# Performance work log

Measured on AMD Instinct MI355X. Metric: run time of the kernel, lower is better.

## Reference

```python
import jax, jax.numpy as jnp
import numpy as np

B = 16           # number of graphs
H = 8            # heads
NC = 9           # num_coeffs = (lmax+1)^2
DM = 128         # d_model (sphere_channels)
F = NC * DM      # flat_dim = 1152
HD = F // H      # head_dim = 144
RD = 16          # rope_dim
EPS = 1e-5


def setup_inputs() -> dict:
    key = jax.random.key(0)
    ks = jax.random.split(key, 8)
    N = 8192
    x_emb = jax.random.normal(ks[0], (N, NC, DM), dtype=jnp.float32)
    batch = jnp.sort(jax.random.randint(ks[1], (N,), 0, B)).astype(jnp.int32)
    pos = jax.random.normal(ks[2], (N, 3), dtype=jnp.float32) * 3.0
    Wqkv = jax.random.normal(ks[3], (F, 3 * F), dtype=jnp.float32) / np.sqrt(F)
    Wout = jax.random.normal(ks[4], (F, F), dtype=jnp.float32) / np.sqrt(F)
    rope_freqs = jax.random.normal(ks[5], (RD,), dtype=jnp.float32) * 0.1
    Wrope = jax.random.normal(ks[6], (RD, H), dtype=jnp.float32) / np.sqrt(RD)
    gamma = jnp.ones((F,), dtype=jnp.float32)
    beta = jnp.zeros((F,), dtype=jnp.float32)
    return {"x_emb": x_emb, "pos": pos, "Wqkv": Wqkv, "Wout": Wout,
            "rope_freqs": rope_freqs, "Wrope": Wrope,
            "gamma": gamma, "beta": beta, "batch": batch}


def _pad_layout(batch, N):
    # sorted batch ids -> per-node rank within its graph, sizes per graph
    sizes = jnp.bincount(batch, length=B)                       # [B]
    offsets = jnp.concatenate([jnp.zeros((1,), sizes.dtype), jnp.cumsum(sizes)[:-1]])
    rank = jnp.arange(N, dtype=sizes.dtype) - offsets[batch]    # [N]
    n_max = int(np.asarray(jax.device_get(sizes)).max())        # concrete pad width
    return sizes, rank, n_max


def reference(x_emb, pos, Wqkv, Wout, rope_freqs, Wrope, gamma, beta, batch):
    N = x_emb.shape[0]
    x_flat = x_emb.reshape(N, F)
    sizes, rank, n_max = _pad_layout(batch, N)

    # dense padding  [B, N_max, *]; mask True = padding slot
    x_pad = jnp.zeros((B, n_max, F), x_flat.dtype).at[batch, rank].set(x_flat)
    pos_pad = jnp.zeros((B, n_max, 3), pos.dtype).at[batch, rank].set(pos)
    mask = jnp.arange(n_max)[None, :] >= sizes[:, None]         # [B, N_max]

    qkv = x_pad @ Wqkv                                          # [B, N_max, 3F]
    q, k, v = jnp.split(qkv, 3, axis=-1)
    def heads(t):
        return t.reshape(B, n_max, H, HD).transpose(0, 2, 1, 3)  # [B,H,N_max,HD]
    q, k, v = heads(q), heads(k), heads(v)

    scale = HD ** (-0.5)
    attn = jnp.einsum('bhid,bhjd->bhij', q, k) * scale          # [B,H,N,N]

    # Fourier distance bias
    diff = pos_pad[:, :, None, :] - pos_pad[:, None, :, :]      # [B,N,N,3]
    dist = jnp.linalg.norm(diff, axis=-1)                       # [B,N,N]
    fourier = jnp.cos(dist[..., None] * jnp.abs(rope_freqs))    # [B,N,N,RD]
    bias = jnp.einsum('bijr,rh->bhij', fourier, Wrope)          # [B,H,N,N]
    pad_mask = mask[:, None, :] | mask[:, :, None]              # [B,N,N]
    bias = jnp.where(pad_mask[:, None, :, :], 0.0, bias)
    attn = attn + bias

    attn = jnp.where(mask[:, None, None, :], -jnp.inf, attn)    # key mask
    attn = jax.nn.softmax(attn, axis=-1)
    attn = jnp.nan_to_num(attn)

    out = jnp.einsum('bhij,bhjd->bhid', attn, v)                # [B,H,N,HD]
    out = out.transpose(0, 2, 1, 3).reshape(B, n_max, F) @ Wout
    out_flat = out[batch, rank]                                 # gather back [N,F]

    h = x_flat + out_flat
    mu = jnp.mean(h, axis=-1, keepdims=True)
    var = jnp.var(h, axis=-1, keepdims=True)
    y = (h - mu) / jnp.sqrt(var + EPS) * gamma + beta
    return y.reshape(N, NC, DM)
```

## Files before the change

kernel.cpp:

```cpp
#include <hip/hip_runtime.h>

typedef unsigned short u16;
typedef unsigned int   u32;
typedef __attribute__((ext_vector_type(8)))  __bf16 bf16x8;
typedef __attribute__((ext_vector_type(4)))  float  f32x4;
typedef __attribute__((ext_vector_type(16))) float  f32x16;
typedef __attribute__((ext_vector_type(4)))  u32    u32x4;

#define F_DIM   1152
#define QKV_DIM 3456
#define HD_SCALE 0.083333333333333333f
#define LOG2E    1.4426950408889634f
#define KSC      (HD_SCALE*LOG2E)
#define MAX4    80
#define BIAS_BLKS 2048

static __device__ __forceinline__ u16 f2bf(float f){
    u32 u = __builtin_bit_cast(u32, f);
    u32 r = u + 0x7fffu + ((u >> 16) & 1u);
    return (u16)(r >> 16);
}
static __device__ __forceinline__ u32 cvtpk(float lo, float hi){
    u32 r;
    asm("v_cvt_pk_bf16_f32 %0, %1, %2" : "=v"(r) : "v"(lo), "v"(hi));
    return r;
}

typedef __attribute__((address_space(1))) void gvoid;
typedef __attribute__((address_space(3))) void lvoid;
static __device__ __forceinline__ void gload16(const u16* g, u16* l){
    __builtin_amdgcn_global_load_lds((gvoid*)g, (lvoid*)l, 16, 0, 0);
}

__global__ __launch_bounds__(256) void prep_kernel(
        const float* __restrict__ x, u16* __restrict__ xb, int nCast, int n4,
        const float* __restrict__ Wqkv, u16* __restrict__ wqkvT,
        const float* __restrict__ Wout, u16* __restrict__ woutT,
        const float* __restrict__ pos, const float* __restrict__ rfreq,
        const float* __restrict__ Wrope, u16* __restrict__ biasP,
        const int* __restrict__ batch, int* __restrict__ meta, int N){
    __shared__ float tile[32][33];
    __shared__ int goffs[17];
    __shared__ int bpre[17];
    const int b = blockIdx.x, t = threadIdx.x;
    const int T1 = (QKV_DIM/32)*(F_DIM/32);
    const int T2 = (F_DIM/32)*(F_DIM/32);

    if (b < BIAS_BLKS){
        if (t <= 16){
            int lo = 0, hi = N;
            while (lo < hi){ int mid = (lo+hi)>>1; if (batch[mid] < t) lo = mid+1; else hi = mid; }
            goffs[t] = lo;
        }
        __syncthreads();
        if (t == 0){
            int bc = 0;
            for (int g = 0; g < 16; g++){
                bpre[g] = bc;
                int ng = goffs[g+1] - goffs[g];
                int ntg = (ng + 31) >> 5;
                bc += ntg*ntg;
            }
            bpre[16] = bc;
        }
        __syncthreads();
        float absf[16], w[16][8];
        #pragma unroll
        for (int r = 0; r < 16; r++){
            absf[r] = fabsf(rfreq[r]);
            #pragma unroll
            for (int h = 0; h < 8; h++) w[r][h] = Wrope[r*8 + h] * LOG2E;
        }
        const int total = bpre[16];
        for (int bb = b; bb < total; bb += BIAS_BLKS){
            int g = 0;
            while (bpre[g+1] <= bb) g++;
            int rem  = bb - bpre[g];
            int goff = goffs[g];
            int ng   = goffs[g+1] - goff;
            int ntg  = (ng + 31) >> 5;
            int qt   = rem / ntg;
            int jt   = rem - qt*ntg;
            size_t base = (size_t)bb * 8192;
            #pragma unroll
            for (int pp = 0; pp < 4; pp++){
                int p = t + pp*256;
                int i = p >> 5, c = p & 31;
                int p4 = c & 15;
                int j  = (p4 & 3) + ((p4 >> 2) << 3) + ((c >> 4) << 2);
                int qn = goff + qt*32 + i;  if (qn >= goff + ng) qn = goff + ng - 1;
                int kn = goff + jt*32 + j;  if (kn >= goff + ng) kn = goff + ng - 1;
                float dx = pos[qn*3+0] - pos[kn*3+0];
                float dy = pos[qn*3+1] - pos[kn*3+1];
                float dz = pos[qn*3+2] - pos[kn*3+2];
                float d  = sqrtf(dx*dx + dy*dy + dz*dz);
                float bv[8];
                #pragma unroll
                for (int h = 0; h < 8; h++) bv[h] = 0.f;
                #pragma unroll
                for (int r = 0; r < 16; r++){
                    float cs = __cosf(d * absf[r]);
                    #pragma unroll
                    for (int h = 0; h < 8; h++) bv[h] = fmaf(cs, w[r][h], bv[h]);
                }
                #pragma unroll
                for (int h = 0; h < 8; h++)
                    biasP[base + h*1024 + p] = f2bf(bv[h]);
            }
        }
        return;
    }
    const int b2 = b - BIAS_BLKS;
    if (b2 < nCast){
        int i = b2*256 + t;
        if (i < n4){
            float4 v = ((const float4*)x)[i];
            ((ushort4*)xb)[i] = make_ushort4(f2bf(v.x), f2bf(v.y), f2bf(v.z), f2bf(v.w));
        }
        return;
    }
    if (b2 < nCast + T1 + T2){
        const float* in; u16* out; int R, C, bi;
        if (b2 < nCast + T1){ in = Wqkv; out = wqkvT; R = F_DIM; C = QKV_DIM; bi = b2 - nCast; }
        else                { in = Wout; out = woutT; R = F_DIM; C = F_DIM;  bi = b2 - nCast - T1; }
        int gx = C/32;
        int c0 = (bi % gx)*32, r0 = (bi / gx)*32;
        int tx = t & 31, ty = t >> 5;
        #pragma unroll
        for (int yy = ty; yy < 32; yy += 8)
            tile[yy][tx] = in[(size_t)(r0+yy)*C + (c0+tx)];
        __syncthreads();
        #pragma unroll
        for (int yy = ty; yy < 32; yy += 8)
            out[(size_t)(c0+yy)*R + (r0+tx)] = f2bf(tile[tx][yy]);
        return;
    }
    if (t <= 16){
        int lo = 0, hi = N;
        while (lo < hi){ int mid = (lo+hi)>>1; if (batch[mid] < t) lo = mid+1; else hi = mid; }
        meta[1+t] = lo;
    }
    __syncthreads();
    if (t == 0){
        int ps = 0, bcnt = 0, cnt4 = 0;
        for (int g = 0; g < 16; g++){
            int ng = meta[2+g] - meta[1+g];
            meta[20+g] = ps;
            meta[40+g] = bcnt;
            int nt = (ng + 31) / 32;
            ps += nt * 32;
            bcnt += nt * nt;
            int nt4 = (nt + 3) / 4;
            for (int q4 = 0; q4 < nt4; q4++){
                meta[64 + cnt4] = g;
                meta[64 + MAX4 + cnt4] = q4;
                cnt4++;
            }
        }
        meta[36] = ps;
        meta[56] = bcnt;
        meta[0]  = cnt4;
    }
}

template<bool OUT_BF16>
__global__ __launch_bounds__(512, 2) void gemm256(const u16* __restrict__ A,
                                                  const u16* __restrict__ Bt,
                                                  void* __restrict__ Cp,
                                                  int M, int Ncols, int K){
    __shared__ u16 sA[4][8192];
    __shared__ u16 sB[4][8192];
    const int nwg = gridDim.x;
    int orig = blockIdx.x;
    int qq = nwg >> 3, rr = nwg & 7;
    int xcd = orig & 7, pos = orig >> 3;
    int nid = (xcd < rr ? xcd*(qq+1) : rr*(qq+1) + (xcd-rr)*qq) + pos;
    const int gx = M >> 8;
    const int bm = (nid % gx) << 8, bn = (nid / gx) << 8;

    const int tid = threadIdx.x;
    const int w = tid >> 6, lane = tid & 63;
    const int wr = w >> 2, wc = w & 3;
    const int fr = lane & 15, fq = lane >> 4;
    const int swz8 = (fq ^ ((fr >> 1) & 3)) * 8;

    const u16* aS[2]; const u16* bS[2]; int dOf[2];
    #pragma unroll
    for (int p = 0; p < 2; p++){
        int idx = p*512 + tid;
        int row = idx >> 2, c = idx & 3;
        int sc = c ^ ((row >> 1) & 3);
        int brow = bn + row; if (brow > Ncols-1) brow = Ncols-1;
        aS[p] = A  + (size_t)(bm + row)*K + sc*8;
        bS[p] = Bt + (size_t)brow*K + sc*8;
        dOf[p] = idx*8;
    }

    f32x4 acc[8][4];
    #pragma unroll
    for (int m = 0; m < 8; m++)
        #pragma unroll
        for (int n = 0; n < 4; n++)
            #pragma unroll
            for (int e = 0; e < 4; e++) acc[m][n][e] = 0.f;

    const int nk = K >> 5;
    #pragma unroll
    for (int p = 0; p < 2; p++){ gload16(aS[p], &sA[0][dOf[p]]); gload16(bS[p], &sB[0][dOf[p]]); }
    #pragma unroll
    for (int p = 0; p < 2; p++){ gload16(aS[p]+32, &sA[1][dOf[p]]); gload16(bS[p]+32, &sB[1][dOf[p]]); }

    #pragma unroll 1
    for (int t = 0; t < nk; t++){
        int tp = (t+2 < nk) ? t+2 : nk-1;
        int bufS = (t+2) & 3;
        #pragma unroll
        for (int p = 0; p < 2; p++){
            gload16(aS[p] + tp*32, &sA[bufS][dOf[p]]);
            gload16(bS[p] + tp*32, &sB[bufS][dOf[p]]);
        }
        asm volatile("s_waitcnt vmcnt(8)\n\ts_barrier" ::: "memory");

        const u16* sAc = &sA[t & 3][0];
        const u16* sBc = &sB[t & 3][0];
        bf16x8 af[8], bfr[4];
        #pragma unroll
        for (int m = 0; m < 8; m++)
            af[m] = *(const bf16x8*)(sAc + (wr*128 + m*16 + fr)*32 + swz8);
        #pragma unroll
        for (int n = 0; n < 4; n++)
            bfr[n] = *(const bf16x8*)(sBc + (wc*64 + n*16 + fr)*32 + swz8);
        __builtin_amdgcn_s_setprio(1);
        #pragma unroll
        for (int m = 0; m < 8; m++)
            #pragma unroll
            for (int n = 0; n < 4; n++)
                acc[m][n] = __builtin_amdgcn_mfma_f32_16x16x32_bf16(af[m], bfr[n], acc[m][n], 0, 0, 0);
        __builtin_amdgcn_s_setprio(0);
    }

    #pragma unroll
    for (int m = 0; m < 8; m++)
        #pragma unroll
        for (int n = 0; n < 4; n++)
            #pragma unroll
            for (int r = 0; r < 4; r++){
                int row = bm + wr*128 + m*16 + fq*4 + r;
                int col = bn + wc*64 + n*16 + fr;
                if (col < Ncols){
                    float v = acc[m][n][r];
                    if (OUT_BF16) ((u16*)Cp)[(size_t)row*Ncols + col] = f2bf(v);
                    else          ((float*)Cp)[(size_t)row*Ncols + col] = v;
                }
            }
}

__global__ __launch_bounds__(256) void pack_v(const u16* __restrict__ qkv,
                                              u16* __restrict__ Vpack,
                                              const int* __restrict__ batch,
                                              const int* __restrict__ meta,
                                              int PT){
    __shared__ u16 tile[32][33];
    int nt0 = blockIdx.x*32, dt0 = blockIdx.y*32, h = blockIdx.z;
    int tx = threadIdx.x & 31, ty = threadIdx.x >> 5;
    #pragma unroll
    for (int yy = ty; yy < 32; yy += 8){
        int node = nt0+yy, d = dt0+tx;
        tile[yy][tx] = (d < 144) ? qkv[(size_t)node*QKV_DIM + 2*F_DIM + h*144 + d] : (u16)0;
    }
    __syncthreads();
    int node = nt0 + tx;
    int g = batch[node];
    int col = meta[20+g] + (node - meta[1+g]);
    int pt = col >> 5, cl = col & 31;
    #pragma unroll
    for (int yy = ty; yy < 32; yy += 8){
        int d = dt0+yy;
        if (d < 144) Vpack[(((size_t)h*PT + pt)*144 + d)*32 + cl] = tile[tx][yy];
    }
}

__global__ __launch_bounds__(256) void attn_kernel(
        const u16* __restrict__ qkv, const u16* __restrict__ Vpack,
        const u16* __restrict__ biasP, u16* __restrict__ attn_out,
        const int* __restrict__ meta, int PT){
    __shared__ u16 sK[2][4864];
    __shared__ u16 sV[2][4608];
    const int h = blockIdx.x & 7, t4 = blockIdx.x >> 3;
    if (t4 >= meta[0]) return;
    const int g    = meta[64 + t4];
    const int q4   = meta[64 + MAX4 + t4];
    const int goff = meta[1+g], gend = meta[2+g];
    const int ng   = gend - goff;
    const int ntg  = (ng + 31) >> 5;
    const int pst  = meta[20+g];
    const int boffg= meta[40+g];

    const int tid = threadIdx.x;
    const int w = tid >> 6, lane = tid & 63;
    const int li = lane & 31, hi = lane >> 5;
    const int qt = q4*4 + w;
    const int qbase = goff + qt*32;
    const int qtP = (qt < ntg) ? qt : (ntg - 1);

    int kOff[3];
    #pragma unroll
    for (int p = 0; p < 3; p++){
        int idx = p*256 + tid;
        if (idx > 607) idx = 607;
        int row = idx/19, c = idx - row*19;
        if (c == 18) c = 0;
        kOff[p] = row*QKV_DIM + c*8;
    }
    const u16* kBase = qkv + (size_t)goff*QKV_DIM + F_DIM + h*144;
    int vOff[3];
    #pragma unroll
    for (int p = 0; p < 3; p++){
        int idx = p*256 + tid;
        if (idx > 575) idx = 575;
        int d = idx >> 2, c = idx & 3;
        vOff[p] = d*32 + ((c ^ (d & 3)) << 3);
    }
    const u16* vBase = Vpack + ((size_t)h*PT + (pst >> 5))*4608;
    const u16* bBase = biasP + ((size_t)boffg + (size_t)qtP*ntg)*8192 + h*1024 + li*32 + hi*16;

    int qnode = qbase + li; if (qnode >= gend) qnode = gend - 1;
    const u16* qrow = qkv + (size_t)qnode*QKV_DIM + h*144;
    bf16x8 qf[9];
    #pragma unroll
    for (int kk = 0; kk < 9; kk++) qf[kk] = *(const bf16x8*)(qrow + kk*16 + hi*8);

    int jlr[16];
    #pragma unroll
    for (int r = 0; r < 16; r++) jlr[r] = (r & 3) + ((r >> 2) << 3) + (hi << 2);

    float lrun = 0.f;
    f32x16 O[5];
    #pragma unroll
    for (int dt = 0; dt < 5; dt++)
        #pragma unroll
        for (int e = 0; e < 16; e++) O[dt][e] = 0.f;

    u32x4 bA0, bA1, bN0, bN1;
    bA0 = *(const u32x4*)bBase;
    bA1 = *(const u32x4*)(bBase + 8);
    {
        gload16(kBase + kOff[0], &sK[0][tid*8]);
        gload16(kBase + kOff[1], &sK[0][(256+tid)*8]);
        if (tid < 96) gload16(kBase + kOff[2], &sK[0][(512+tid)*8]);
        gload16(vBase + vOff[0], &sV[0][tid*8]);
        gload16(vBase + vOff[1], &sV[0][(256+tid)*8]);
        if (tid < 64) gload16(vBase + vOff[2], &sV[0][(512+tid)*8]);
    }
    __syncthreads();

    #pragma unroll 1
    for (int t = 0; t < ntg; t++){
        const int cur = t & 1;
        int tn = (t+1 < ntg) ? t+1 : ntg-1;
        bN0 = *(const u32x4*)(bBase + (size_t)tn*8192);
        bN1 = *(const u32x4*)(bBase + (size_t)tn*8192 + 8);
        __builtin_amdgcn_sched_barrier(0);
        if (t+1 < ntg){
            const u16* kb = kBase + (size_t)(t+1)*32*QKV_DIM;
            const u16* vb = vBase + (size_t)(t+1)*4608;
            gload16(kb + kOff[0], &sK[cur^1][tid*8]);
            gload16(kb + kOff[1], &sK[cur^1][(256+tid)*8]);
            if (tid < 96) gload16(kb + kOff[2], &sK[cur^1][(512+tid)*8]);
            gload16(vb + vOff[0], &sV[cur^1][tid*8]);
            gload16(vb + vOff[1], &sV[cur^1][(256+tid)*8]);
            if (tid < 64) gload16(vb + vOff[2], &sV[cur^1][(512+tid)*8]);
        }

        const u16* sKc = &sK[cur][0];
        f32x16 sacc;
        #pragma unroll
        for (int e = 0; e < 16; e++) sacc[e] = 0.f;
        __builtin_amdgcn_s_setprio(1);
        #pragma unroll
        for (int kk = 0; kk < 9; kk++){
            bf16x8 kf = *(const bf16x8*)(sKc + li*152 + kk*16 + hi*8);
            sacc = __builtin_amdgcn_mfma_f32_32x32x16_bf16(kf, qf[kk], sacc, 0, 0, 0);
        }
        __builtin_amdgcn_s_setprio(0);

        float bfv[16];
        #pragma unroll
        for (int q = 0; q < 4; q++){
            bfv[2*q]     = __builtin_bit_cast(float, bA0[q] << 16);
            bfv[2*q+1]   = __builtin_bit_cast(float, bA0[q] & 0xffff0000u);
            bfv[8+2*q]   = __builtin_bit_cast(float, bA1[q] << 16);
            bfv[8+2*q+1] = __builtin_bit_cast(float, bA1[q] & 0xffff0000u);
        }

        const int j0 = t*32;
        float p[16];
        float psum = 0.f;
        if (j0 + 32 <= ng){
            #pragma unroll
            for (int r = 0; r < 16; r++){
                float s_ = fminf(fmaf(sacc[r], KSC, bfv[r]), 86.f);
                p[r] = exp2f(s_); psum += p[r];
            }
        } else {
            #pragma unroll
            for (int r = 0; r < 16; r++){
                float s_ = fminf(fmaf(sacc[r], KSC, bfv[r]), 86.f);
                p[r] = (j0 + jlr[r] < ng) ? exp2f(s_) : 0.f;
                psum += p[r];
            }
        }
        psum += __shfl_xor(psum, 32);
        lrun += psum;

        u32 cpk[8], opk[8];
        #pragma unroll
        for (int q = 0; q < 8; q++) cpk[q] = cvtpk(p[2*q], p[2*q+1]);
        #pragma unroll
        for (int q = 0; q < 8; q++) opk[q] = (u32)__shfl_xor((int)cpk[q], 32);
        u32x4 a0, a1;
        if (hi == 0){
            a0[0]=cpk[0]; a0[1]=cpk[1]; a0[2]=opk[0]; a0[3]=opk[1];
            a1[0]=cpk[4]; a1[1]=cpk[5]; a1[2]=opk[4]; a1[3]=opk[5];
        } else {
            a0[0]=opk[2]; a0[1]=opk[3]; a0[2]=cpk[2]; a0[3]=cpk[3];
            a1[0]=opk[6]; a1[1]=opk[7]; a1[2]=cpk[6]; a1[3]=cpk[7];
        }
        bf16x8 paf0 = __builtin_bit_cast(bf16x8, a0);
        bf16x8 paf1 = __builtin_bit_cast(bf16x8, a1);

        const u16* sVc = &sV[cur][0];
        __builtin_amdgcn_s_setprio(1);
        #pragma unroll
        for (int dt = 0; dt < 5; dt++){
            int d = dt*32 + li;
            int dc = (d > 143) ? 143 : d;
            int swzlo = ((hi     ^ (dc & 3)) << 3);
            int swzhi = (((2+hi) ^ (dc & 3)) << 3);
            bf16x8 v0 = *(const bf16x8*)(sVc + dc*32 + swzlo);
            bf16x8 v1 = *(const bf16x8*)(sVc + dc*32 + swzhi);
            O[dt] = __builtin_amdgcn_mfma_f32_32x32x16_bf16(paf0, v0, O[dt], 0, 0, 0);
            O[dt] = __builtin_amdgcn_mfma_f32_32x32x16_bf16(paf1, v1, O[dt], 0, 0, 0);
        }
        __builtin_amdgcn_s_setprio(0);

        bA0 = bN0; bA1 = bN1;
        __syncthreads();
    }

    if (qt < ntg){
        float lr[16];
        #pragma unroll
        for (int r = 0; r < 16; r++) lr[r] = 1.0f / __shfl(lrun, jlr[r]);
        #pragma unroll
        for (int dt = 0; dt < 5; dt++){
            int d = dt*32 + li;
            if (d < 144){
                #pragma unroll
                for (int r = 0; r < 16; r++){
                    int qi = jlr[r];
                    if (qt*32 + qi < ng)
                        attn_out[(size_t)(qbase + qi)*F_DIM + h*144 + d] = f2bf(O[dt][r]*lr[r]);
                }
            }
        }
    }
}

__global__ __launch_bounds__(256) void ln_kernel(const float* __restrict__ x,
                                                 float* __restrict__ io,
                                                 const float* __restrict__ gamma,
                                                 const float* __restrict__ beta){
    const int node = blockIdx.x;
    const float* xr = x  + (size_t)node*F_DIM;
    float* yr       = io + (size_t)node*F_DIM;
    const int t = threadIdx.x;
    float h[5]; float s = 0.f, ss = 0.f;
    #pragma unroll
    for (int i = 0; i < 5; i++){
        int idx = t + i*256;
        float v = 0.f;
        if (idx < F_DIM) v = xr[idx] + yr[idx];
        h[i] = v; s += v; ss += v*v;
    }
    #pragma unroll
    for (int o = 32; o > 0; o >>= 1){ s += __shfl_down(s, o); ss += __shfl_down(ss, o); }
    __shared__ float rs[4], rss[4];
    __shared__ float smu, srstd;
    if ((t & 63) == 0){ rs[t>>6] = s; rss[t>>6] = ss; }
    __syncthreads();
    if (t == 0){
        float S  = rs[0]+rs[1]+rs[2]+rs[3];
        float SS = rss[0]+rss[1]+rss[2]+rss[3];
        float mu = S * (1.f/F_DIM);
        float var = SS * (1.f/F_DIM) - mu*mu;
        smu = mu; srstd = rsqrtf(var + 1e-5f);
    }
    __syncthreads();
    float mu = smu, rstd = srstd;
    #pragma unroll
    for (int i = 0; i < 5; i++){
        int idx = t + i*256;
        if (idx < F_DIM) yr[idx] = (h[i]-mu)*rstd*gamma[idx] + beta[idx];
    }
}

extern "C" void kernel_launch(void* const* d_in, const int* in_sizes, int n_in,
                              void* d_out, int out_size, void* d_ws, size_t ws_size,
                              hipStream_t stream){
    const float* x     = (const float*)d_in[0];
    const float* pos   = (const float*)d_in[1];
    const float* Wqkv  = (const float*)d_in[2];
    const float* Wout  = (const float*)d_in[3];
    const float* rfreq = (const float*)d_in[4];
    const float* Wrope = (const float*)d_in[5];
    const float* gamma = (const float*)d_in[6];
    const float* beta  = (const float*)d_in[7];
    const int*   batch = (const int*)d_in[8];

    const int N  = in_sizes[0] / F_DIM;
    const int PN = N + 512;
    const int PT = PN / 32;

    char* ws = (char*)d_ws;
    size_t off = 0;
    auto alloc = [&](size_t b){ size_t o = off; off += (b + 255) & ~(size_t)255; return o; };
    int* meta   = (int*)(ws + alloc((size_t)(64 + 2*MAX4 + 64)*sizeof(int)));
    u16* xb     = (u16*)(ws + alloc((size_t)N*F_DIM*2));
    u16* wqkvT  = (u16*)(ws + alloc((size_t)QKV_DIM*F_DIM*2));
    u16* woutT  = (u16*)(ws + alloc((size_t)F_DIM*F_DIM*2));
    u16* qkv    = (u16*)(ws + alloc((size_t)N*QKV_DIM*2));
    u16* Vpack  = (u16*)(ws + alloc((size_t)8*PT*144*32*2));
    u16* biasb  = (u16*)(ws + off);
    (void)ws_size; (void)n_in; (void)out_size;

    const int n4    = N*F_DIM/4;
    const int nCast = (n4 + 255)/256;
    const int nT    = (QKV_DIM/32)*(F_DIM/32) + (F_DIM/32)*(F_DIM/32);
    hipLaunchKernelGGL(prep_kernel, dim3(BIAS_BLKS + nCast + nT + 1), dim3(256), 0, stream,
                       x, xb, nCast, n4, Wqkv, wqkvT, Wout, woutT,
                       pos, rfreq, Wrope, biasb, batch, meta, N);
    hipLaunchKernelGGL((gemm256<true>), dim3((N/256)*((QKV_DIM+255)/256)), dim3(512), 0, stream,
                       xb, wqkvT, (void*)qkv, N, QKV_DIM, F_DIM);
    hipLaunchKernelGGL(pack_v, dim3(N/32, 5, 8), dim3(256), 0, stream,
                       qkv, Vpack, batch, meta, PT);
    hipLaunchKernelGGL(attn_kernel, dim3(MAX4*8), dim3(256), 0, stream,
                       qkv, Vpack, biasb, xb, meta, PT);
    hipLaunchKernelGGL((gemm256<false>), dim3((N/256)*((F_DIM+255)/256)), dim3(512), 0, stream,
                       xb, woutT, d_out, N, F_DIM, F_DIM);
    hipLaunchKernelGGL(ln_kernel, dim3(N), dim3(256), 0, stream,
                       x, (float*)d_out, gamma, beta);
}
```

Baseline: 287.5 us.

## Restructure GEMM to 1024-thread double-buffered tiles and interleave prep blocks

The GEMM moves from 512 threads with 8x4 MFMA tiles per wave and a 4-stage LDS ring to 1024 threads with 4x4 tiles per wave and a 2-stage buffer. A second barrier is added before each slot is refilled. This halves LDS per block and the accumulator registers per wave, aiming for more waves in flight, but it cuts prefetch depth and adds a sync per K step. The prep kernel spreads the distance-bias blocks one in every four block IDs so they mix with the cast and transpose blocks, and each cast thread now converts four float4 values.

```diff
diff --git a/kernel.cpp b/kernel.cpp
--- a/kernel.cpp
+++ b/kernel.cpp
@@ -33,7 +33,7 @@
 }
 
 __global__ __launch_bounds__(256) void prep_kernel(
-        const float* __restrict__ x, u16* __restrict__ xb, int nCast, int n4,
+        const float* __restrict__ x, u16* __restrict__ xb, int n4,
         const float* __restrict__ Wqkv, u16* __restrict__ wqkvT,
         const float* __restrict__ Wout, u16* __restrict__ woutT,
         const float* __restrict__ pos, const float* __restrict__ rfreq,
@@ -44,9 +44,11 @@
     __shared__ int bpre[17];
     const int b = blockIdx.x, t = threadIdx.x;
     const int T1 = (QKV_DIM/32)*(F_DIM/32);
-    const int T2 = (F_DIM/32)*(F_DIM/32);
-
-    if (b < BIAS_BLKS){
+    const int NC4 = 2304;
+
+    bool isBias = (b < 8192) && ((b & 3) == 0);
+    if (isBias){
+        const int bidx = b >> 2;
         if (t <= 16){
             int lo = 0, hi = N;
             while (lo < hi){ int mid = (lo+hi)>>1; if (batch[mid] < t) lo = mid+1; else hi = mid; }
@@ -72,7 +74,7 @@
             for (int h = 0; h < 8; h++) w[r][h] = Wrope[r*8 + h] * LOG2E;
         }
         const int total = bpre[16];
-        for (int bb = b; bb < total; bb += BIAS_BLKS){
+        for (int bb = bidx; bb < total; bb += BIAS_BLKS){
             int g = 0;
             while (bpre[g+1] <= bb) g++;
             int rem  = bb - bpre[g];
@@ -110,19 +112,23 @@
         }
         return;
     }
-    const int b2 = b - BIAS_BLKS;
-    if (b2 < nCast){
-        int i = b2*256 + t;
-        if (i < n4){
-            float4 v = ((const float4*)x)[i];
-            ((ushort4*)xb)[i] = make_ushort4(f2bf(v.x), f2bf(v.y), f2bf(v.z), f2bf(v.w));
+    const int mi = (b < 8192) ? (3*(b >> 2) + (b & 3) - 1) : (6144 + (b - 8192));
+    if (mi < NC4){
+        int base = mi*1024 + t;
+        #pragma unroll
+        for (int k = 0; k < 4; k++){
+            int i = base + k*256;
+            if (i < n4){
+                float4 v = ((const float4*)x)[i];
+                ((ushort4*)xb)[i] = make_ushort4(f2bf(v.x), f2bf(v.y), f2bf(v.z), f2bf(v.w));
+            }
         }
         return;
     }
-    if (b2 < nCast + T1 + T2){
+    if (mi < NC4 + T1 + (F_DIM/32)*(F_DIM/32)){
         const float* in; u16* out; int R, C, bi;
-        if (b2 < nCast + T1){ in = Wqkv; out = wqkvT; R = F_DIM; C = QKV_DIM; bi = b2 - nCast; }
-        else                { in = Wout; out = woutT; R = F_DIM; C = F_DIM;  bi = b2 - nCast - T1; }
+        if (mi < NC4 + T1){ in = Wqkv; out = wqkvT; R = F_DIM; C = QKV_DIM; bi = mi - NC4; }
+        else              { in = Wout; out = woutT; R = F_DIM; C = F_DIM;  bi = mi - NC4 - T1; }
         int gx = C/32;
         int c0 = (bi % gx)*32, r0 = (bi / gx)*32;
         int tx = t & 31, ty = t >> 5;
@@ -164,12 +170,12 @@
 }
 
 template<bool OUT_BF16>
-__global__ __launch_bounds__(512, 2) void gemm256(const u16* __restrict__ A,
-                                                  const u16* __restrict__ Bt,
-                                                  void* __restrict__ Cp,
-                                                  int M, int Ncols, int K){
-    __shared__ u16 sA[4][8192];
-    __shared__ u16 sB[4][8192];
+__global__ __launch_bounds__(1024, 2) void gemm256(const u16* __restrict__ A,
+                                                   const u16* __restrict__ Bt,
+                                                   void* __restrict__ Cp,
+                                                   int M, int Ncols, int K){
+    __shared__ u16 sA[2][8192];
+    __shared__ u16 sB[2][8192];
     const int nwg = gridDim.x;
     int orig = blockIdx.x;
     int qq = nwg >> 3, rr = nwg & 7;
@@ -184,68 +190,59 @@
     const int fr = lane & 15, fq = lane >> 4;
     const int swz8 = (fq ^ ((fr >> 1) & 3)) * 8;
 
-    const u16* aS[2]; const u16* bS[2]; int dOf[2];
-    #pragma unroll
-    for (int p = 0; p < 2; p++){
-        int idx = p*512 + tid;
-        int row = idx >> 2, c = idx & 3;
-        int sc = c ^ ((row >> 1) & 3);
-        int brow = bn + row; if (brow > Ncols-1) brow = Ncols-1;
-        aS[p] = A  + (size_t)(bm + row)*K + sc*8;
-        bS[p] = Bt + (size_t)brow*K + sc*8;
-        dOf[p] = idx*8;
-    }
-
-    f32x4 acc[8][4];
-    #pragma unroll
-    for (int m = 0; m < 8; m++)
+    const int srow = tid >> 2, sc0 = tid & 3;
+    const int sc = sc0 ^ ((srow >> 1) & 3);
+    int brow = bn + srow; if (brow > Ncols-1) brow = Ncols-1;
+    const u16* aS = A  + (size_t)(bm + srow)*K + sc*8;
+    const u16* bS = Bt + (size_t)brow*K + sc*8;
+    const int dOf = tid*8;
+
+    f32x4 acc[4][4];
+    #pragma unroll
+    for (int m = 0; m < 4; m++)
         #pragma unroll
         for (int n = 0; n < 4; n++)
             #pragma unroll
             for (int e = 0; e < 4; e++) acc[m][n][e] = 0.f;
 
     const int nk = K >> 5;
-    #pragma unroll
-    for (int p = 0; p < 2; p++){ gload16(aS[p], &sA[0][dOf[p]]); gload16(bS[p], &sB[0][dOf[p]]); }
-    #pragma unroll
-    for (int p = 0; p < 2; p++){ gload16(aS[p]+32, &sA[1][dOf[p]]); gload16(bS[p]+32, &sB[1][dOf[p]]); }
+    gload16(aS,      &sA[0][dOf]);
+    gload16(bS,      &sB[0][dOf]);
+    gload16(aS + 32, &sA[1][dOf]);
+    gload16(bS + 32, &sB[1][dOf]);
 
     #pragma unroll 1
     for (int t = 0; t < nk; t++){
-        int tp = (t+2 < nk) ? t+2 : nk-1;
-        int bufS = (t+2) & 3;
-        #pragma unroll
-        for (int p = 0; p < 2; p++){
-            gload16(aS[p] + tp*32, &sA[bufS][dOf[p]]);
-            gload16(bS[p] + tp*32, &sB[bufS][dOf[p]]);
-        }
-        asm volatile("s_waitcnt vmcnt(8)\n\ts_barrier" ::: "memory");
-
-        const u16* sAc = &sA[t & 3][0];
-        const u16* sBc = &sB[t & 3][0];
-        bf16x8 af[8], bfr[4];
-        #pragma unroll
-        for (int m = 0; m < 8; m++)
-            af[m] = *(const bf16x8*)(sAc + (wr*128 + m*16 + fr)*32 + swz8);
+        asm volatile("s_waitcnt vmcnt(2)\n\ts_barrier" ::: "memory");
+        const u16* sAc = &sA[t & 1][0];
+        const u16* sBc = &sB[t & 1][0];
+        bf16x8 af[4], bfr[4];
+        #pragma unroll
+        for (int m = 0; m < 4; m++)
+            af[m] = *(const bf16x8*)(sAc + (wr*64 + m*16 + fr)*32 + swz8);
         #pragma unroll
         for (int n = 0; n < 4; n++)
             bfr[n] = *(const bf16x8*)(sBc + (wc*64 + n*16 + fr)*32 + swz8);
         __builtin_amdgcn_s_setprio(1);
         #pragma unroll
-        for (int m = 0; m < 8; m++)
+        for (int m = 0; m < 4; m++)
             #pragma unroll
             for (int n = 0; n < 4; n++)
                 acc[m][n] = __builtin_amdgcn_mfma_f32_16x16x32_bf16(af[m], bfr[n], acc[m][n], 0, 0, 0);
         __builtin_amdgcn_s_setprio(0);
-    }
-
-    #pragma unroll
-    for (int m = 0; m < 8; m++)
+        asm volatile("s_waitcnt lgkmcnt(0)\n\ts_barrier" ::: "memory");
+        int tp = (t+2 < nk) ? t+2 : nk-1;
+        gload16(aS + tp*32, &sA[t & 1][dOf]);
+        gload16(bS + tp*32, &sB[t & 1][dOf]);
+    }
+
+    #pragma unroll
+    for (int m = 0; m < 4; m++)
         #pragma unroll
         for (int n = 0; n < 4; n++)
             #pragma unroll
             for (int r = 0; r < 4; r++){
-                int row = bm + wr*128 + m*16 + fq*4 + r;
+                int row = bm + wr*64 + m*16 + fq*4 + r;
                 int col = bn + wc*64 + n*16 + fr;
                 if (col < Ncols){
                     float v = acc[m][n][r];
@@ -534,19 +531,17 @@
     u16* biasb  = (u16*)(ws + off);
     (void)ws_size; (void)n_in; (void)out_size;
 
-    const int n4    = N*F_DIM/4;
-    const int nCast = (n4 + 255)/256;
-    const int nT    = (QKV_DIM/32)*(F_DIM/32) + (F_DIM/32)*(F_DIM/32);
-    hipLaunchKernelGGL(prep_kernel, dim3(BIAS_BLKS + nCast + nT + 1), dim3(256), 0, stream,
-                       x, xb, nCast, n4, Wqkv, wqkvT, Wout, woutT,
+    const int n4 = N*F_DIM/4;
+    hipLaunchKernelGGL(prep_kernel, dim3(9537), dim3(256), 0, stream,
+                       x, xb, n4, Wqkv, wqkvT, Wout, woutT,
                        pos, rfreq, Wrope, biasb, batch, meta, N);
-    hipLaunchKernelGGL((gemm256<true>), dim3((N/256)*((QKV_DIM+255)/256)), dim3(512), 0, stream,
+    hipLaunchKernelGGL((gemm256<true>), dim3((N/256)*((QKV_DIM+255)/256)), dim3(1024), 0, stream,
                        xb, wqkvT, (void*)qkv, N, QKV_DIM, F_DIM);
     hipLaunchKernelGGL(pack_v, dim3(N/32, 5, 8), dim3(256), 0, stream,
                        qkv, Vpack, batch, meta, PT);
     hipLaunchKernelGGL(attn_kernel, dim3(MAX4*8), dim3(256), 0, stream,
                        qkv, Vpack, biasb, xb, meta, PT);
-    hipLaunchKernelGGL((gemm256<false>), dim3((N/256)*((F_DIM+255)/256)), dim3(512), 0, stream,
+    hipLaunchKernelGGL((gemm256<false>), dim3((N/256)*((F_DIM+255)/256)), dim3(1024), 0, stream,
                        xb, woutT, d_out, N, F_DIM, F_DIM);
     hipLaunchKernelGGL(ln_kernel, dim3(N), dim3(256), 0, stream,
                        x, (float*)d_out, gamma, beta);
```

Result: slower. 358.9 us (+24.8%).
